# Kernel optimization log

Measured on AMD Instinct MI355X. Metric: run time of the kernel, lower is better.

Reference implementation:

```python
import jax, jax.numpy as jnp
import numpy as np

B, D, L, K = 262144, 64, 4, 8
BOUND = 3.0
MIN_BW = 1e-3   # min bin width
MIN_BH = 1e-3   # min bin height
MIN_D = 1e-3    # min derivative
MIN_LAM = 0.025 # min lambda
EPS = 1e-6


def _knots(lengths, lo, hi):
    # lengths: (D, K) normalized bin fractions -> (bin lengths (D,K), knot positions (D,K+1))
    knots = jnp.cumsum(lengths, axis=-1)
    knots = jnp.pad(knots, ((0, 0), (1, 0)))
    knots = (hi - lo) * knots + lo
    knots = knots.at[..., 0].set(lo)
    knots = knots.at[..., -1].set(hi)
    return knots[..., 1:] - knots[..., :-1], knots


def _gather(p, idx):
    # p: (D, K'), idx: (B, D) -> (B, D): per-dimension bin-parameter gather
    return p[jnp.arange(p.shape[0])[None, :], idx]


def spline_layer(x, uw, uh, ud, ul):
    # x: (B, D); uw/uh/ul: (D, K); ud: (D, K-1). Linear-order monotonic rational spline (pyro).
    w = jax.nn.softmax(uw, axis=-1)
    h = jax.nn.softmax(uh, axis=-1)
    d = jax.nn.softplus(ud)
    lam = jax.nn.sigmoid(ul)

    num_bins = w.shape[-1]
    left, right = -BOUND, BOUND
    inside = (x >= left) & (x <= right)
    xc = jnp.clip(x, left, right)  # identity applied outside; clamp keeps inside-branch math finite

    w = MIN_BW + (1.0 - MIN_BW * num_bins) * w
    h = MIN_BH + (1.0 - MIN_BH * num_bins) * h
    d = MIN_D + d
    widths, cumw = _knots(w, left, right)
    heights, cumh = _knots(h, left, right)
    d = jnp.pad(d, ((0, 0), (1, 1)), constant_values=1.0)  # boundary derivatives fixed to 1
    lam = (1.0 - 2.0 * MIN_LAM) * lam + MIN_LAM

    # data-dependent bin search (searchsorted via comparison-sum, as in pyro)
    bin_idx = jnp.sum(xc[..., None] >= (cumw + EPS)[None], axis=-1) - 1  # (B, D)
    bin_idx = jnp.clip(bin_idx, 0, num_bins - 1)

    iw = _gather(widths, bin_idx)
    icw = _gather(cumw, bin_idx)
    ich = _gather(cumh, bin_idx)
    idelta = _gather(heights / widths, bin_idx)
    id0 = _gather(d[:, :-1], bin_idx)
    id1 = _gather(d[:, 1:], bin_idx)
    ih = _gather(heights, bin_idx)
    il = _gather(lam, bin_idx)

    wa = 1.0
    wb = jnp.sqrt(id0 / id1) * wa
    wc = (il * wa * id0 + (1.0 - il) * wb * id1) / idelta
    ya = ich
    yb = ih + ich
    yc = ((1.0 - il) * wa * ya + il * wb * yb) / ((1.0 - il) * wa + il * wb)

    theta = (xc - icw) / iw
    lower = theta <= il
    num = jnp.where(lower, wa * ya * (il - theta) + wc * yc * theta,
                    wc * yc * (1.0 - theta) + wb * yb * (theta - il))
    den = jnp.where(lower, wa * (il - theta) + wc * theta,
                    wc * (1.0 - theta) + wb * (theta - il))
    out = num / den
    dnum = jnp.where(lower, wa * wc * il * (yc - ya), wb * wc * (1.0 - il) * (yb - yc)) / iw
    lad = jnp.log(dnum) - 2.0 * jnp.log(jnp.abs(den))

    out = jnp.where(inside, out, x)
    lad = jnp.where(inside, lad, 0.0)
    return out, jnp.sum(lad, axis=1)


def setup_inputs() -> dict:
    key = jax.random.key(0)
    k0, k1, k2, k3, k4 = jax.random.split(key, 5)
    return {
        "x": jax.random.normal(k0, (B, D), dtype=jnp.float32),
        "uw": jax.random.normal(k1, (L, D, K), dtype=jnp.float32),
        "uh": jax.random.normal(k2, (L, D, K), dtype=jnp.float32),
        "ud": jax.random.normal(k3, (L, D, K - 1), dtype=jnp.float32),
        "ul": jax.random.uniform(k4, (L, D, K), dtype=jnp.float32),
    }


def reference(x, uw, uh, ud, ul):
    def step(carry, params):
        xi, ld = carry
        pw, ph, pd, pl = params
        xi, l = spline_layer(xi, pw, ph, pd, pl)
        return (xi, ld + l), None
    init = (x, jnp.zeros(x.shape[0], x.dtype))
    (x, log_det), _ = jax.lax.scan(step, init, (uw, uh, ud, ul))
    return x, log_det
```

## Files before the change

### kernel.cpp

```cpp
#include <hip/hip_runtime.h>


#define BATCH 262144
#define DIM   64
#define NLAY  4
#define NK    8

#define OFF_KN0 0
#define OFF_KN1 2048
#define OFF_CRS 4096
#define OFF_CF0 4544

__device__ __forceinline__ void softmax_knots(const float* p, float minb,
                                              float* kn, float* len) {
  float v[NK];
  float m = p[0];
  for (int k = 1; k < NK; ++k) m = fmaxf(m, p[k]);
  float s = 0.f;
  for (int k = 0; k < NK; ++k) { v[k] = expf(p[k] - m); s += v[k]; }
  float invs = 1.f / s;
  for (int k = 0; k < NK; ++k) v[k] = minb + (1.f - minb * (float)NK) * (v[k] * invs);
  kn[0] = -3.f;
  float c = 0.f;
  for (int k = 0; k < NK; ++k) { c += v[k]; kn[k+1] = 6.f * c - 3.f; }
  kn[NK] = 3.f;
  for (int k = 0; k < NK; ++k) len[k] = kn[k+1] - kn[k];
}

__global__ void nf_pre(const float* __restrict__ uw, const float* __restrict__ uh,
                       const float* __restrict__ ud, const float* __restrict__ ul,
                       float* __restrict__ F) {
  __shared__ double Lb[NLAY][17], Ly[NLAY][17], LM[NLAY][16][4], Ld[NLAY][16];
  __shared__ double sx[64], Fb[65];
  int d = blockIdx.x;
  int t = threadIdx.x;

  if (t < NLAY) {
    int l = t;
    const float* pw  = uw + (l*DIM + d)*NK;
    const float* ph  = uh + (l*DIM + d)*NK;
    const float* pdv = ud + (l*DIM + d)*(NK-1);
    const float* pl  = ul + (l*DIM + d)*NK;
    float kw[NK+1], ww[NK], kh[NK+1], hh[NK], dv[NK+1], lm[NK];
    softmax_knots(pw, 1e-3f, kw, ww);
    softmax_knots(ph, 1e-3f, kh, hh);
    dv[0] = 1.f; dv[NK] = 1.f;
    for (int k = 0; k < NK-1; ++k) {
      float u = pdv[k];
      dv[k+1] = 1e-3f + (fmaxf(u, 0.f) + log1pf(expf(-fabsf(u))));
    }
    for (int k = 0; k < NK; ++k) {
      float sg = 1.f / (1.f + expf(-pl[k]));
      lm[k] = 0.95f * sg + 0.025f;
    }
    Lb[l][0] = -3.0; Lb[l][16] = 3.0;
    Ly[l][0] = -3.0; Ly[l][16] = 3.0;
    for (int k = 0; k < NK; ++k) {
      float delta = hh[k] / ww[k];
      float wbf = sqrtf(dv[k] / dv[k+1]);
      float wcf = (lm[k]*dv[k] + (1.f-lm[k])*wbf*dv[k+1]) / delta;
      float yaf = kh[k], ybf = hh[k] + kh[k];
      float ycf = ((1.f-lm[k])*yaf + lm[k]*wbf*ybf) / ((1.f-lm[k]) + lm[k]*wbf);
      if (k) Lb[l][2*k] = (double)(kw[k] + 1.0e-6f);
      Lb[l][2*k+1] = (double)kw[k] + (double)lm[k]*(double)ww[k];
      Ly[l][2*k]   = (double)yaf;
      Ly[l][2*k+1] = (double)ycf;
      double icw = (double)kw[k], iw = (double)ww[k], il = (double)lm[k];
      double wb = wbf, wc = wcf, ya = yaf, yb = ybf, yc = ycf;
      double n0 = ya*il, n1 = wc*yc - ya, d0 = il, d1 = wc - 1.0;
      double A = n1, Bv = n0*iw - n1*icw, C = d1, Dv = d0*iw - d1*icw;
      LM[l][2*k][0]=A; LM[l][2*k][1]=Bv; LM[l][2*k][2]=C; LM[l][2*k][3]=Dv;
      Ld[l][2*k] = log2(A*Dv - Bv*C);
      n0 = wc*yc - il*wb*yb; n1 = wb*yb - wc*yc; d0 = wc - il*wb; d1 = wb - wc;
      A = n1; Bv = n0*iw - n1*icw; C = d1; Dv = d0*iw - d1*icw;
      LM[l][2*k+1][0]=A; LM[l][2*k+1][1]=Bv; LM[l][2*k+1][2]=C; LM[l][2*k+1][3]=Dv;
      Ld[l][2*k+1] = log2(A*Dv - Bv*C);
    }
  }
  __syncthreads();

  if (t < 60) {
    int lp  = t / 15;
    int mth = t % 15 + 1;
    double x = Lb[lp][mth];
    for (int q = lp - 1; q >= 0; --q) {
      int j = 0;
      for (int k = 1; k <= 15; ++k) j += (x >= Ly[q][k]) ? 1 : 0;
      const double* M = LM[q][j];
      x = (M[3]*x - M[1]) / (M[0] - M[2]*x);
    }
    sx[t] = x;
  }
  __syncthreads();
  if (t < 60) {
    double x = sx[t];
    int r = 0;
    for (int s2 = 0; s2 < 60; ++s2) {
      double o = sx[s2];
      r += (o < x || (o == x && s2 < t)) ? 1 : 0;
    }
    Fb[r+1] = x;
  }
  if (t == 0)  Fb[0] = -3.0;
  if (t >= 60) Fb[t+1] = 3.0;
  __syncthreads();

  {
    int j = t;
    float bf;
    if (j == 0)       bf = -3.0f;
    else if (j <= 60) bf = (float)Fb[j];
    else              bf = 1e30f;
    int cw = j >> 3, r8 = j & 7;
    if (r8 < 4) F[OFF_KN0 + (cw*DIM + d)*4 + r8]     = bf;
    else        F[OFF_KN1 + (cw*DIM + d)*4 + (r8-4)] = bf;
    if (j >= 8 && (j & 7) == 0 && j <= 56) F[OFF_CRS + (j/8 - 1)*DIM + d] = bf;
  }

  if (t < 61) {
    int p = t;
    double bl = Fb[p], br = Fb[p+1];
    float xmf = (float)(0.5*(bl+br));
    xmf = fminf(fmaxf(xmf, -3.f), 3.f);
    double y = (double)xmf;
    double A=1.0, Bv=0.0, C=0.0, Dv=1.0, ld2 = 0.0;
    for (int q = 0; q < NLAY; ++q) {
      int j = 0;
      for (int k = 1; k <= 15; ++k) j += (y >= Lb[q][k]) ? 1 : 0;
      const double* M = LM[q][j];
      ld2 += Ld[q][j];
      double A2 = M[0]*A + M[1]*C, B2 = M[0]*Bv + M[1]*Dv;
      double C2 = M[2]*A + M[3]*C, D2 = M[2]*Bv + M[3]*Dv;
      y = (M[0]*y + M[1]) / (M[2]*y + M[3]);
      A=A2; Bv=B2; C=C2; Dv=D2;
    }
    double sinv = exp2(-0.5 * ld2);
    float4 c4;
    c4.x = (float)(A*sinv); c4.y = (float)(Bv*sinv);
    c4.z = (float)(C*sinv); c4.w = (float)(Dv*sinv);
    *(float4*)(F + OFF_CF0 + (size_t)(p*DIM + d)*4) = c4;
  }
}

template <int CTRL>
__device__ __forceinline__ float dpp_add(float x) {
  int yi = __builtin_amdgcn_update_dpp(0, __float_as_int(x), CTRL, 0xF, 0xF, false);
  return x + __int_as_float(yi);
}
__device__ __forceinline__ float wave_sum63(float x) {
  x = dpp_add<0x111>(x);
  x = dpp_add<0x112>(x);
  x = dpp_add<0x114>(x);
  x = dpp_add<0x118>(x);
  x = dpp_add<0x142>(x);
  x = dpp_add<0x143>(x);
  return x;
}

__global__ __launch_bounds__(1024, 4) void nf_main(const float* __restrict__ X,
                                                   const float* __restrict__ F,
                                                   float* __restrict__ OUT,
                                                   float* __restrict__ LDo) {
  __shared__ float smem[19712];
  int t = threadIdx.x;
  {
    float4* dst = (float4*)smem;
    const float4* kt = (const float4*)(F + OFF_KN0);
    dst[t] = kt[t];
    const float4* ct = (const float4*)(F + OFF_CF0);
    for (int i = t; i < 3904; i += 1024) dst[1024 + i] = ct[i];
  }
  int d = t & 63;
  float k1 = F[OFF_CRS + 0*DIM + d];
  float k2 = F[OFF_CRS + 1*DIM + d];
  float k3 = F[OFF_CRS + 2*DIM + d];
  float k4 = F[OFF_CRS + 3*DIM + d];
  float k5 = F[OFF_CRS + 4*DIM + d];
  float k6 = F[OFF_CRS + 5*DIM + d];
  float k7 = F[OFF_CRS + 6*DIM + d];
  __syncthreads();
  const float4* skv = (const float4*)smem;

  int gw = blockIdx.x * 16 + (t >> 6);
  const float* Xb = X   + (size_t)gw*32*DIM + d;
  float*       Ob = OUT + (size_t)gw*32*DIM + d;
  float*       Lp = LDo + (size_t)gw*32;

#define COARSE(xc) ((xc>=k1)+(xc>=k2)+(xc>=k3)+(xc>=k4)+(xc>=k5)+(xc>=k6)+(xc>=k7))
#define FINE(xc, cc, f0, f1) \
  ((cc<<3) + (int)(xc>=f0.y)+(int)(xc>=f0.z)+(int)(xc>=f0.w)+(int)(xc>=f1.x) \
           + (int)(xc>=f1.y)+(int)(xc>=f1.z)+(int)(xc>=f1.w))

  float xA0 = Xb[0], xA1 = Xb[64];
  float xB0 = Xb[128], xB1 = Xb[192];
  float xcA0 = fminf(fmaxf(xA0, -3.f), 3.f);
  float xcA1 = fminf(fmaxf(xA1, -3.f), 3.f);
  float4 cfA0, cfA1;
  {
    int c0 = COARSE(xcA0), c1 = COARSE(xcA1);
    float4 f00 = skv[(c0<<6)+d], f01 = skv[512+(c0<<6)+d];
    float4 f10 = skv[(c1<<6)+d], f11 = skv[512+(c1<<6)+d];
    int p0 = FINE(xcA0, c0, f00, f01);
    int p1 = FINE(xcA1, c1, f10, f11);
    cfA0 = skv[1024+(p0<<6)+d];
    cfA1 = skv[1024+(p1<<6)+d];
  }

#pragma unroll 3
  for (int it = 0; it < 15; ++it) {
    float xcB0 = fminf(fmaxf(xB0, -3.f), 3.f);
    float xcB1 = fminf(fmaxf(xB1, -3.f), 3.f);
    int cB0 = COARSE(xcB0), cB1 = COARSE(xcB1);
    float4 f00 = skv[(cB0<<6)+d], f01 = skv[512+(cB0<<6)+d];
    float4 f10 = skv[(cB1<<6)+d], f11 = skv[512+(cB1<<6)+d];
    int u2 = (it < 14) ? (it + 2) : 15;
    float xF0 = Xb[u2*128], xF1 = Xb[u2*128 + 64];
    __builtin_amdgcn_sched_barrier(0);
    float num0 = fmaf(cfA0.x, xcA0, cfA0.y);
    float den0 = fmaf(cfA0.z, xcA0, cfA0.w);
    float o0 = (xA0 == xcA0) ? __fdividef(num0, den0) : xA0;
    float l0 = -1.3862943611198906f * __log2f(fabsf(den0));
    float num1 = fmaf(cfA1.x, xcA1, cfA1.y);
    float den1 = fmaf(cfA1.z, xcA1, cfA1.w);
    float o1 = (xA1 == xcA1) ? __fdividef(num1, den1) : xA1;
    float l1 = -1.3862943611198906f * __log2f(fabsf(den1));
    Ob[it*128] = o0; Ob[it*128 + 64] = o1;
    float s0 = wave_sum63(l0);
    float s1 = wave_sum63(l1);
    if (d == 63) {
      float2 v; v.x = s0; v.y = s1;
      *(float2*)(Lp + 2*it) = v;
    }
    __builtin_amdgcn_sched_barrier(0);
    int p0 = FINE(xcB0, cB0, f00, f01);
    int p1 = FINE(xcB1, cB1, f10, f11);
    cfA0 = skv[1024+(p0<<6)+d];
    cfA1 = skv[1024+(p1<<6)+d];
    xA0 = xB0; xA1 = xB1; xcA0 = xcB0; xcA1 = xcB1;
    xB0 = xF0; xB1 = xF1;
  }
  {
    float num0 = fmaf(cfA0.x, xcA0, cfA0.y);
    float den0 = fmaf(cfA0.z, xcA0, cfA0.w);
    float o0 = (xA0 == xcA0) ? __fdividef(num0, den0) : xA0;
    float l0 = -1.3862943611198906f * __log2f(fabsf(den0));
    float num1 = fmaf(cfA1.x, xcA1, cfA1.y);
    float den1 = fmaf(cfA1.z, xcA1, cfA1.w);
    float o1 = (xA1 == xcA1) ? __fdividef(num1, den1) : xA1;
    float l1 = -1.3862943611198906f * __log2f(fabsf(den1));
    Ob[15*128] = o0; Ob[15*128 + 64] = o1;
    float s0 = wave_sum63(l0);
    float s1 = wave_sum63(l1);
    if (d == 63) {
      float2 v; v.x = s0; v.y = s1;
      *(float2*)(Lp + 30) = v;
    }
  }
#undef COARSE
#undef FINE
}

extern "C" void kernel_launch(void* const* d_in, const int* in_sizes, int n_in,
                              void* d_out, int out_size, void* d_ws, size_t ws_size,
                              hipStream_t stream) {
  const float* x  = (const float*)d_in[0];
  const float* uw = (const float*)d_in[1];
  const float* uh = (const float*)d_in[2];
  const float* ud = (const float*)d_in[3];
  const float* ul = (const float*)d_in[4];
  float* out = (float*)d_out;
  float* F = (float*)d_ws;
  nf_pre<<<DIM, 64, 0, stream>>>(uw, uh, ud, ul, F);
  nf_main<<<512, 1024, 0, stream>>>(x, F, out, out + (size_t)BATCH*DIM);
}
```

Baseline: 51.78 us.

## Parallelize spline precompute per bin and read fine knots from global memory

The precompute kernel now uses 32 threads, one per (layer, bin), instead of 4 serial threads, to shorten its critical path. The main kernel no longer stages the fine-knot tables in LDS and reads them straight from global memory (served by cache). It raises the launch-bound occupancy hint from 4 to 8 and removes the unroll-3 pragma. The goal is less shared memory per block and higher occupancy, at the cost of extra global/L1 gathers in the inner loop.

Result: slower. 54.43 us (+5.1%).

```diff
diff --git a/kernel.cpp b/kernel.cpp
--- a/kernel.cpp
+++ b/kernel.cpp
@@ -10,22 +10,6 @@
 #define OFF_KN1 2048
 #define OFF_CRS 4096
 #define OFF_CF0 4544
-
-__device__ __forceinline__ void softmax_knots(const float* p, float minb,
-                                              float* kn, float* len) {
-  float v[NK];
-  float m = p[0];
-  for (int k = 1; k < NK; ++k) m = fmaxf(m, p[k]);
-  float s = 0.f;
-  for (int k = 0; k < NK; ++k) { v[k] = expf(p[k] - m); s += v[k]; }
-  float invs = 1.f / s;
-  for (int k = 0; k < NK; ++k) v[k] = minb + (1.f - minb * (float)NK) * (v[k] * invs);
-  kn[0] = -3.f;
-  float c = 0.f;
-  for (int k = 0; k < NK; ++k) { c += v[k]; kn[k+1] = 6.f * c - 3.f; }
-  kn[NK] = 3.f;
-  for (int k = 0; k < NK; ++k) len[k] = kn[k+1] - kn[k];
-}
 
 __global__ void nf_pre(const float* __restrict__ uw, const float* __restrict__ uh,
                        const float* __restrict__ ud, const float* __restrict__ ul,
@@ -35,47 +19,75 @@
   int d = blockIdx.x;
   int t = threadIdx.x;
 
-  if (t < NLAY) {
-    int l = t;
+  if (t < 32) {
+    int l = t >> 3, k = t & 7;
     const float* pw  = uw + (l*DIM + d)*NK;
     const float* ph  = uh + (l*DIM + d)*NK;
     const float* pdv = ud + (l*DIM + d)*(NK-1);
     const float* pl  = ul + (l*DIM + d)*NK;
-    float kw[NK+1], ww[NK], kh[NK+1], hh[NK], dv[NK+1], lm[NK];
-    softmax_knots(pw, 1e-3f, kw, ww);
-    softmax_knots(ph, 1e-3f, kh, hh);
-    dv[0] = 1.f; dv[NK] = 1.f;
-    for (int k = 0; k < NK-1; ++k) {
-      float u = pdv[k];
-      dv[k+1] = 1e-3f + (fmaxf(u, 0.f) + log1pf(expf(-fabsf(u))));
-    }
-    for (int k = 0; k < NK; ++k) {
-      float sg = 1.f / (1.f + expf(-pl[k]));
-      lm[k] = 0.95f * sg + 0.025f;
-    }
-    Lb[l][0] = -3.0; Lb[l][16] = 3.0;
-    Ly[l][0] = -3.0; Ly[l][16] = 3.0;
-    for (int k = 0; k < NK; ++k) {
-      float delta = hh[k] / ww[k];
-      float wbf = sqrtf(dv[k] / dv[k+1]);
-      float wcf = (lm[k]*dv[k] + (1.f-lm[k])*wbf*dv[k+1]) / delta;
-      float yaf = kh[k], ybf = hh[k] + kh[k];
-      float ycf = ((1.f-lm[k])*yaf + lm[k]*wbf*ybf) / ((1.f-lm[k]) + lm[k]*wbf);
-      if (k) Lb[l][2*k] = (double)(kw[k] + 1.0e-6f);
-      Lb[l][2*k+1] = (double)kw[k] + (double)lm[k]*(double)ww[k];
-      Ly[l][2*k]   = (double)yaf;
-      Ly[l][2*k+1] = (double)ycf;
-      double icw = (double)kw[k], iw = (double)ww[k], il = (double)lm[k];
-      double wb = wbf, wc = wcf, ya = yaf, yb = ybf, yc = ycf;
-      double n0 = ya*il, n1 = wc*yc - ya, d0 = il, d1 = wc - 1.0;
-      double A = n1, Bv = n0*iw - n1*icw, C = d1, Dv = d0*iw - d1*icw;
-      LM[l][2*k][0]=A; LM[l][2*k][1]=Bv; LM[l][2*k][2]=C; LM[l][2*k][3]=Dv;
-      Ld[l][2*k] = log2(A*Dv - Bv*C);
-      n0 = wc*yc - il*wb*yb; n1 = wb*yb - wc*yc; d0 = wc - il*wb; d1 = wb - wc;
-      A = n1; Bv = n0*iw - n1*icw; C = d1; Dv = d0*iw - d1*icw;
-      LM[l][2*k+1][0]=A; LM[l][2*k+1][1]=Bv; LM[l][2*k+1][2]=C; LM[l][2*k+1][3]=Dv;
-      Ld[l][2*k+1] = log2(A*Dv - Bv*C);
-    }
+
+    float ev[NK];
+    float mw = pw[0];
+    for (int j = 1; j < NK; ++j) mw = fmaxf(mw, pw[j]);
+    float sw = 0.f;
+    for (int j = 0; j < NK; ++j) { ev[j] = expf(pw[j] - mw); sw += ev[j]; }
+    float invw = 1.f / sw;
+    float cwe = 0.f, cwi = 0.f;
+    for (int j = 0; j <= k; ++j) {
+      float vj = 1e-3f + (1.f - 1e-3f * (float)NK) * (ev[j] * invw);
+      cwe = cwi; cwi += vj;
+    }
+    float kwL = (k == 0) ? -3.f : 6.f * cwe - 3.f;
+    float kwR = (k == 7) ?  3.f : 6.f * cwi - 3.f;
+    float wwk = kwR - kwL;
+
+    float mh = ph[0];
+    for (int j = 1; j < NK; ++j) mh = fmaxf(mh, ph[j]);
+    float sh = 0.f;
+    for (int j = 0; j < NK; ++j) { ev[j] = expf(ph[j] - mh); sh += ev[j]; }
+    float invh = 1.f / sh;
+    float che = 0.f, chi = 0.f;
+    for (int j = 0; j <= k; ++j) {
+      float vj = 1e-3f + (1.f - 1e-3f * (float)NK) * (ev[j] * invh);
+      che = chi; chi += vj;
+    }
+    float khL = (k == 0) ? -3.f : 6.f * che - 3.f;
+    float khR = (k == 7) ?  3.f : 6.f * chi - 3.f;
+    float hhk = khR - khL;
+
+    float dvk, dvk1;
+    if (k == 0) dvk = 1.f;
+    else { float u = pdv[k-1]; dvk  = 1e-3f + (fmaxf(u,0.f) + log1pf(expf(-fabsf(u)))); }
+    if (k == 7) dvk1 = 1.f;
+    else { float u = pdv[k];   dvk1 = 1e-3f + (fmaxf(u,0.f) + log1pf(expf(-fabsf(u)))); }
+    float sg = 1.f / (1.f + expf(-pl[k]));
+    float lmk = 0.95f * sg + 0.025f;
+
+    float delta = hhk / wwk;
+    float wbf = sqrtf(dvk / dvk1);
+    float wcf = (lmk*dvk + (1.f-lmk)*wbf*dvk1) / delta;
+    float yaf = khL, ybf = hhk + khL;
+    float ycf = ((1.f-lmk)*yaf + lmk*wbf*ybf) / ((1.f-lmk) + lmk*wbf);
+
+    if (k == 0) {
+      Lb[l][0] = -3.0; Lb[l][16] = 3.0;
+      Ly[l][0] = -3.0; Ly[l][16] = 3.0;
+    }
+    if (k) Lb[l][2*k] = (double)(kwL + 1.0e-6f);
+    Lb[l][2*k+1] = (double)kwL + (double)lmk*(double)wwk;
+    Ly[l][2*k]   = (double)yaf;
+    Ly[l][2*k+1] = (double)ycf;
+
+    double icw = (double)kwL, iw = (double)wwk, il = (double)lmk;
+    double wb = wbf, wc = wcf, ya = yaf, yb = ybf, yc = ycf;
+    double n0 = ya*il, n1 = wc*yc - ya, d0 = il, d1 = wc - 1.0;
+    double A = n1, Bv = n0*iw - n1*icw, C = d1, Dv = d0*iw - d1*icw;
+    LM[l][2*k][0]=A; LM[l][2*k][1]=Bv; LM[l][2*k][2]=C; LM[l][2*k][3]=Dv;
+    Ld[l][2*k] = log2(A*Dv - Bv*C);
+    n0 = wc*yc - il*wb*yb; n1 = wb*yb - wc*yc; d0 = wc - il*wb; d1 = wb - wc;
+    A = n1; Bv = n0*iw - n1*icw; C = d1; Dv = d0*iw - d1*icw;
+    LM[l][2*k+1][0]=A; LM[l][2*k+1][1]=Bv; LM[l][2*k+1][2]=C; LM[l][2*k+1][3]=Dv;
+    Ld[l][2*k+1] = log2(A*Dv - Bv*C);
   }
   __syncthreads();
 
@@ -157,18 +169,16 @@
   return x;
 }
 
-__global__ __launch_bounds__(1024, 4) void nf_main(const float* __restrict__ X,
+__global__ __launch_bounds__(1024, 8) void nf_main(const float* __restrict__ X,
                                                    const float* __restrict__ F,
                                                    float* __restrict__ OUT,
                                                    float* __restrict__ LDo) {
-  __shared__ float smem[19712];
+  __shared__ float smem[15616];
   int t = threadIdx.x;
   {
     float4* dst = (float4*)smem;
-    const float4* kt = (const float4*)(F + OFF_KN0);
-    dst[t] = kt[t];
     const float4* ct = (const float4*)(F + OFF_CF0);
-    for (int i = t; i < 3904; i += 1024) dst[1024 + i] = ct[i];
+    for (int i = t; i < 3904; i += 1024) dst[i] = ct[i];
   }
   int d = t & 63;
   float k1 = F[OFF_CRS + 0*DIM + d];
@@ -180,6 +190,8 @@
   float k7 = F[OFF_CRS + 6*DIM + d];
   __syncthreads();
   const float4* skv = (const float4*)smem;
+  const float4* KT0 = (const float4*)(F + OFF_KN0);
+  const float4* KT1 = (const float4*)(F + OFF_KN1);
 
   int gw = blockIdx.x * 16 + (t >> 6);
   const float* Xb = X   + (size_t)gw*32*DIM + d;
@@ -198,21 +210,20 @@
   float4 cfA0, cfA1;
   {
     int c0 = COARSE(xcA0), c1 = COARSE(xcA1);
-    float4 f00 = skv[(c0<<6)+d], f01 = skv[512+(c0<<6)+d];
-    float4 f10 = skv[(c1<<6)+d], f11 = skv[512+(c1<<6)+d];
+    float4 f00 = KT0[(c0<<6)+d], f01 = KT1[(c0<<6)+d];
+    float4 f10 = KT0[(c1<<6)+d], f11 = KT1[(c1<<6)+d];
     int p0 = FINE(xcA0, c0, f00, f01);
     int p1 = FINE(xcA1, c1, f10, f11);
-    cfA0 = skv[1024+(p0<<6)+d];
-    cfA1 = skv[1024+(p1<<6)+d];
-  }
-
-#pragma unroll 3
+    cfA0 = skv[(p0<<6)+d];
+    cfA1 = skv[(p1<<6)+d];
+  }
+
   for (int it = 0; it < 15; ++it) {
     float xcB0 = fminf(fmaxf(xB0, -3.f), 3.f);
     float xcB1 = fminf(fmaxf(xB1, -3.f), 3.f);
     int cB0 = COARSE(xcB0), cB1 = COARSE(xcB1);
-    float4 f00 = skv[(cB0<<6)+d], f01 = skv[512+(cB0<<6)+d];
-    float4 f10 = skv[(cB1<<6)+d], f11 = skv[512+(cB1<<6)+d];
+    float4 f00 = KT0[(cB0<<6)+d], f01 = KT1[(cB0<<6)+d];
+    float4 f10 = KT0[(cB1<<6)+d], f11 = KT1[(cB1<<6)+d];
     int u2 = (it < 14) ? (it + 2) : 15;
     float xF0 = Xb[u2*128], xF1 = Xb[u2*128 + 64];
     __builtin_amdgcn_sched_barrier(0);
@@ -234,8 +245,8 @@
     __builtin_amdgcn_sched_barrier(0);
     int p0 = FINE(xcB0, cB0, f00, f01);
     int p1 = FINE(xcB1, cB1, f10, f11);
-    cfA0 = skv[1024+(p0<<6)+d];
-    cfA1 = skv[1024+(p1<<6)+d];
+    cfA0 = skv[(p0<<6)+d];
+    cfA1 = skv[(p1<<6)+d];
     xA0 = xB0; xA1 = xB1; xcA0 = xcB0; xcA1 = xcB1;
     xB0 = xF0; xB1 = xF1;
   }
```
